# Performance work log

Measured on AMD Instinct MI355X. Metric: run time of the kernel, lower is better.

The kernel has to match this reference:

```python
import jax, jax.numpy as jnp
import numpy as np

B, N, D = 512, 256, 16   # batch, tokens (num_patches+1), embed_dim (= n_qubits)
STAGES = 4               # log2(D) butterfly stages


def _safe_acos(u):
    # matches torch acos + nan_to_num: out-of-range -> 0, with clean gradients
    ok = jnp.abs(u) <= 1.0
    return jnp.where(ok, jnp.arccos(jnp.clip(u, -1.0, 1.0)), 0.0)


def get_rbs_parameters(x):
    # x: [B, N, D] -> RBS angles [B, N, D-1]; recursive spherical-coordinate decomposition
    a0 = _safe_acos(x[..., 0])
    def step(carry, xi):
        t, a_prev = carry
        inv = jnp.nan_to_num(1.0 / jnp.sin(a_prev))
        t = t * inv
        a = _safe_acos(xi * t)
        return (t, a), a
    xs = jnp.moveaxis(x[..., 1:D - 1], -1, 0)  # [D-2, B, N]
    _, rest = jax.lax.scan(step, (jnp.ones_like(a0), a0), xs)
    alphas = jnp.concatenate([a0[None], rest], axis=0)  # [D-1, B, N]
    return jnp.moveaxis(alphas, 0, -1)


def amplitudes(alphas):
    # unary-state amplitudes prepared by the diagonal vector loader
    # a_i = cos(alpha_i) * prod_{k<i} sin(alpha_k);  a_{D-1} = prod_k sin(alpha_k)
    sins = jnp.sin(alphas)
    prefix = jnp.concatenate([jnp.ones_like(sins[..., :1]), jnp.cumprod(sins, axis=-1)], axis=-1)  # [B,N,D]
    return jnp.concatenate([prefix[..., :D - 1] * jnp.cos(alphas), prefix[..., D - 1:]], axis=-1)


def butterfly_matrix(angles):
    # orthogonal DxD matrix implemented by the Butterfly RBS circuit in the unary subspace
    d = 2 * angles.shape[1]
    M = jnp.eye(d, dtype=angles.dtype)
    for s in range(angles.shape[0]):
        step = 1 << s
        idx_i = np.array([i for i in range(d) if (i // step) % 2 == 0])
        idx_j = idx_i + step
        c = jnp.cos(angles[s])[:, None]
        sn = jnp.sin(angles[s])[:, None]
        Mi, Mj = M[idx_i], M[idx_j]
        M = M.at[idx_i].set(c * Mi + sn * Mj)
        M = M.at[idx_j].set(-sn * Mi + c * Mj)
    return M


def layer_norm(x, g, b, eps=1e-5):
    mu = jnp.mean(x, -1, keepdims=True)
    var = jnp.var(x, -1, keepdims=True)
    return (x - mu) / jnp.sqrt(var + eps) * g + b


def setup_inputs() -> dict:
    key = jax.random.key(0)
    ks = jax.random.split(key, 4)
    return {
        "x": jax.random.normal(ks[0], (B, N, D), jnp.float32),
        "ln1_g": jnp.ones((D,), jnp.float32),
        "ln1_b": jnp.zeros((D,), jnp.float32),
        "angles": jax.random.normal(ks[1], (STAGES, D // 2), jnp.float32),
        "ln2_g": jnp.ones((D,), jnp.float32),
        "ln2_b": jnp.zeros((D,), jnp.float32),
        "w1": jax.random.normal(ks[2], (D, 4 * D), jnp.float32) / np.sqrt(D).astype(np.float32),
        "b1": jnp.zeros((4 * D,), jnp.float32),
        "w2": jax.random.normal(ks[3], (4 * D, D), jnp.float32) / np.sqrt(4 * D).astype(np.float32),
        "b2": jnp.zeros((D,), jnp.float32),
    }


def reference(x, ln1_g, ln1_b, angles, ln2_g, ln2_b, w1, b1, w2, b2):
    inp = layer_norm(x, ln1_g, ln1_b) / 2.0
    alphas = jnp.nan_to_num(get_rbs_parameters(inp))
    a = amplitudes(alphas)                 # [B,N,D] loaded unary amplitudes
    W = butterfly_matrix(angles)           # [D,D] orthogonal butterfly
    Wa = jnp.einsum('de,bne->bnd', W, a)   # [B,N,D]
    vxT = jnp.abs(Wa)
    # xwx[b,i,j] = sqrt(P(qubit0=1)) = |<a_j| W |a_i>| for the xWx circuit
    xwx = jnp.abs(jnp.einsum('bid,bjd->bij', Wa, a))
    attn = jax.nn.softmax(xwx, axis=-1)
    x = x + jnp.einsum('bij,bjd->bid', attn, vxT)
    h = layer_norm(x, ln2_g, ln2_b)
    h = jax.nn.gelu(h @ w1 + b1, approximate=False) @ w2 + b2
    return x + h
```

## Files before the change

### kernel.cpp

```cpp
#include <hip/hip_runtime.h>
#include <math.h>

#define NTOK 256
#define DD 16
#define BDIM 512

typedef short short8 __attribute__((ext_vector_type(8)));
typedef float f32x16 __attribute__((ext_vector_type(16)));
typedef unsigned int u32;
typedef unsigned long long u64;

__device__ __forceinline__ u32 f2bf(float f) {
    u32 u = __float_as_uint(f);
    u += 0x7FFFu + ((u >> 16) & 1u);
    return u >> 16;
}
struct U128 { u64 a, b; };
__device__ __forceinline__ short8 ld8(const unsigned short* p) {
    U128 t;
    t.a = *(const u64*)(p);
    t.b = *(const u64*)(p + 4);
    return __builtin_bit_cast(short8, t);
}
__device__ __forceinline__ void pack_swap16(f32x16 p, short8& f0, short8& f1) {
    u32 W00, W01, W10, W11, W20, W21, W30, W31;
    asm("v_cvt_pk_bf16_f32 %0, %1, %2" : "=v"(W00) : "v"(p[0]),  "v"(p[1]));
    asm("v_cvt_pk_bf16_f32 %0, %1, %2" : "=v"(W01) : "v"(p[2]),  "v"(p[3]));
    asm("v_cvt_pk_bf16_f32 %0, %1, %2" : "=v"(W10) : "v"(p[4]),  "v"(p[5]));
    asm("v_cvt_pk_bf16_f32 %0, %1, %2" : "=v"(W11) : "v"(p[6]),  "v"(p[7]));
    asm("v_cvt_pk_bf16_f32 %0, %1, %2" : "=v"(W20) : "v"(p[8]),  "v"(p[9]));
    asm("v_cvt_pk_bf16_f32 %0, %1, %2" : "=v"(W21) : "v"(p[10]), "v"(p[11]));
    asm("v_cvt_pk_bf16_f32 %0, %1, %2" : "=v"(W30) : "v"(p[12]), "v"(p[13]));
    asm("v_cvt_pk_bf16_f32 %0, %1, %2" : "=v"(W31) : "v"(p[14]), "v"(p[15]));
    asm("v_permlane32_swap_b32 %0, %1" : "+v"(W00), "+v"(W10));
    asm("v_permlane32_swap_b32 %0, %1" : "+v"(W01), "+v"(W11));
    asm("v_permlane32_swap_b32 %0, %1" : "+v"(W20), "+v"(W30));
    asm("v_permlane32_swap_b32 %0, %1" : "+v"(W21), "+v"(W31));
    struct { u32 x, y, z, w; } i0{W00, W01, W10, W11}, i1{W20, W21, W30, W31};
    f0 = __builtin_bit_cast(short8, i0);
    f1 = __builtin_bit_cast(short8, i1);
}
__device__ __forceinline__ float gelu_erf(float v) {
    float xx = v * 0.70710678118654752f;
    float ax = fabsf(xx);
    float t = __builtin_amdgcn_rcpf(__builtin_fmaf(0.3275911f, ax, 1.0f));
    float poly = t * (0.254829592f + t * (-0.284496736f + t * (1.421413741f
               + t * (-1.453152027f + t * 1.061405429f))));
    float r = 1.0f - poly * __expf(-ax * ax);
    float e = copysignf(r, xx);
    return 0.5f * v * (1.0f + e);
}

__global__ __launch_bounds__(BDIM, 4) void qab_kernel(
    const float* __restrict__ x,
    const float* __restrict__ ln1_g, const float* __restrict__ ln1_b,
    const float* __restrict__ angles,
    const float* __restrict__ ln2_g, const float* __restrict__ ln2_b,
    const float* __restrict__ w1, const float* __restrict__ b1,
    const float* __restrict__ w2, const float* __restrict__ b2,
    float* __restrict__ out)
{
    __shared__ alignas(16) unsigned short a_bf[NTOK][20];
    __shared__ alignas(16) unsigned short wa_bf[NTOK][20];
    __shared__ alignas(16) unsigned short vxT[17][268];
    __shared__ alignas(16) unsigned short w1tb[64][20];
    __shared__ alignas(16) unsigned short w2tb[16][68];
    __shared__ alignas(16) float b1_lds[64];
    __shared__ alignas(16) float ln2g_lds[DD];
    __shared__ alignas(16) float ln2b_lds[DD];
    __shared__ alignas(16) float b2_lds[DD];

    const int b    = blockIdx.x;
    const int tid  = threadIdx.x;
    const int r    = tid & (NTOK - 1);
    const int q    = tid >> 8;
    const int w    = tid >> 6;
    const int l31  = tid & 31;
    const int hi   = (tid >> 5) & 1;
    const int lane = tid & 63;

    const float* xres = x + ((size_t)b * NTOK + 32 * w + l31) * DD;
    const float4 xra = *(const float4*)(xres + 4 * hi);
    const float4 xrb = *(const float4*)(xres + 8 + 4 * hi);

    f32x16 zc;
    #pragma unroll
    for (int t = 0; t < 16; ++t) zc[t] = 0.0f;

    float amp[DD];
    {
        const float* xrow = x + ((size_t)b * NTOK + r) * DD;
        float xr[DD];
        #pragma unroll
        for (int qq = 0; qq < 4; ++qq) {
            float4 v = ((const float4*)xrow)[qq];
            xr[4*qq+0] = v.x; xr[4*qq+1] = v.y; xr[4*qq+2] = v.z; xr[4*qq+3] = v.w;
        }
        float mu = 0.0f;
        #pragma unroll
        for (int d = 0; d < DD; ++d) mu += xr[d];
        mu *= (1.0f / DD);
        float var = 0.0f;
        #pragma unroll
        for (int d = 0; d < DD; ++d) { float dv = xr[d] - mu; var += dv * dv; }
        var *= (1.0f / DD);
        float rs = 1.0f / sqrtf(var + 1e-5f);
        float inp[DD];
        #pragma unroll
        for (int d = 0; d < DD; ++d)
            inp[d] = ((xr[d] - mu) * rs * ln1_g[d] + ln1_b[d]) * 0.5f;

        float P = 1.0f;
        #pragma unroll
        for (int i = 0; i < DD - 1; ++i) {
            float v = inp[i];
            float v2 = v * v;
            bool ok = v2 <= P;
            amp[i] = ok ? v : __builtin_amdgcn_sqrtf(P);
            P = ok ? __builtin_fmaf(-v, v, P) : 0.0f;
        }
        amp[DD - 1] = __builtin_amdgcn_sqrtf(P);
    }

    if (q == 0) {
        u32 aw[8];
        #pragma unroll
        for (int k = 0; k < 8; ++k)
            asm("v_cvt_pk_bf16_f32 %0, %1, %2" : "=v"(aw[k]) : "v"(amp[2*k]), "v"(amp[2*k+1]));
        *(u64*)&a_bf[r][0]  = (u64)aw[0] | ((u64)aw[1] << 32);
        *(u64*)&a_bf[r][4]  = (u64)aw[2] | ((u64)aw[3] << 32);
        *(u64*)&a_bf[r][8]  = (u64)aw[4] | ((u64)aw[5] << 32);
        *(u64*)&a_bf[r][12] = (u64)aw[6] | ((u64)aw[7] << 32);
        for (int i = r; i < 64 * DD; i += NTOK) {
            w1tb[i & 63][i >> 6] = (unsigned short)f2bf(w1[i]);
            w2tb[i & 15][i >> 4] = (unsigned short)f2bf(w2[i]);
        }
        if (r >= 128 && r < 192) b1_lds[r - 128] = b1[r - 128];
        if (r >= 192 && r < 208) ln2g_lds[r - 192] = ln2_g[r - 192];
        if (r >= 208 && r < 224) ln2b_lds[r - 208] = ln2_b[r - 208];
        if (r >= 224 && r < 240) b2_lds[r - 224] = b2[r - 224];
        vxT[16][r] = 0x3F80;
    } else {
        float sn_l = 0.0f, cs_l = 0.0f;
        if (lane < 32) __sincosf(angles[lane], &sn_l, &cs_l);
        #pragma unroll
        for (int s = 0; s < 4; ++s) {
            const int step = 1 << s;
            #pragma unroll
            for (int p = 0; p < 8; ++p) {
                const int i = ((p >> s) << (s + 1)) | (p & (step - 1));
                const int j = i + step;
                float sn = __shfl(sn_l, s * 8 + p, 64);
                float cs = __shfl(cs_l, s * 8 + p, 64);
                float vi = amp[i], vj = amp[j];
                amp[i] =  cs * vi + sn * vj;
                amp[j] = -sn * vi + cs * vj;
            }
        }
        u32 ww[8];
        #pragma unroll
        for (int k = 0; k < 8; ++k)
            asm("v_cvt_pk_bf16_f32 %0, %1, %2" : "=v"(ww[k]) : "v"(amp[2*k]), "v"(amp[2*k+1]));
        *(u64*)&wa_bf[r][0]  = (u64)ww[0] | ((u64)ww[1] << 32);
        *(u64*)&wa_bf[r][4]  = (u64)ww[2] | ((u64)ww[3] << 32);
        *(u64*)&wa_bf[r][8]  = (u64)ww[4] | ((u64)ww[5] << 32);
        *(u64*)&wa_bf[r][12] = (u64)ww[6] | ((u64)ww[7] << 32);
        #pragma unroll
        for (int d = 0; d < DD; ++d)
            vxT[d][r] = (unsigned short)f2bf(fabsf(amp[d]));
    }
    __syncthreads();

    const int ncl = (l31 < 16) ? l31 : 16;
    f32x16 Oacc = zc;
    {
        short8 waf = ld8(&wa_bf[w * 32 + l31][8 * hi]);
        short8 af[8];
        #pragma unroll
        for (int jt = 0; jt < 8; ++jt)
            af[jt] = ld8(&a_bf[jt * 32 + l31][8 * hi]);
        short8 va0 = ld8(&vxT[ncl][8 * hi]);
        short8 va1 = ld8(&vxT[ncl][16 + 8 * hi]);
        f32x16 S0 = __builtin_amdgcn_mfma_f32_32x32x16_bf16(af[0], waf, zc, 0, 0, 0);
        #pragma unroll
        for (int jt = 0; jt < 8; ++jt) {
            f32x16 Sn;
            if (jt < 7)
                Sn = __builtin_amdgcn_mfma_f32_32x32x16_bf16(af[jt + 1], waf, zc, 0, 0, 0);
            short8 nva0, nva1;
            if (jt < 7) {
                nva0 = ld8(&vxT[ncl][(jt + 1) * 32 + 8 * hi]);
                nva1 = ld8(&vxT[ncl][(jt + 1) * 32 + 16 + 8 * hi]);
            }
            f32x16 pv;
            #pragma unroll
            for (int t = 0; t < 16; ++t) pv[t] = __expf(fabsf(S0[t]));
            short8 pb0, pb1;
            pack_swap16(pv, pb0, pb1);
            Oacc = __builtin_amdgcn_mfma_f32_32x32x16_bf16(va0, pb0, Oacc, 0, 0, 0);
            Oacc = __builtin_amdgcn_mfma_f32_32x32x16_bf16(va1, pb1, Oacc, 0, 0, 0);
            S0 = Sn; va0 = nva0; va1 = nva1;
        }
    }

    const float rl = 1.0f / Oacc[8];
    float o1[8];
    o1[0] = xra.x + Oacc[0] * rl;  o1[1] = xra.y + Oacc[1] * rl;
    o1[2] = xra.z + Oacc[2] * rl;  o1[3] = xra.w + Oacc[3] * rl;
    o1[4] = xrb.x + Oacc[4] * rl;  o1[5] = xrb.y + Oacc[5] * rl;
    o1[6] = xrb.z + Oacc[6] * rl;  o1[7] = xrb.w + Oacc[7] * rl;

    float s8 = 0.0f;
    #pragma unroll
    for (int t = 0; t < 8; ++t) s8 += o1[t];
    float mu2 = (s8 + __shfl_xor(s8, 32, 64)) * (1.0f / DD);
    float v8 = 0.0f;
    #pragma unroll
    for (int t = 0; t < 8; ++t) { float dv = o1[t] - mu2; v8 += dv * dv; }
    float var2 = (v8 + __shfl_xor(v8, 32, 64)) * (1.0f / DD);
    float rs2 = 1.0f / sqrtf(var2 + 1e-5f);

    const float4 g0v = *(const float4*)&ln2g_lds[4 * hi];
    const float4 g1v = *(const float4*)&ln2g_lds[8 + 4 * hi];
    const float4 bb0 = *(const float4*)&ln2b_lds[4 * hi];
    const float4 bb1 = *(const float4*)&ln2b_lds[8 + 4 * hi];
    float h[8];
    h[0] = (o1[0]-mu2)*rs2*g0v.x + bb0.x;  h[1] = (o1[1]-mu2)*rs2*g0v.y + bb0.y;
    h[2] = (o1[2]-mu2)*rs2*g0v.z + bb0.z;  h[3] = (o1[3]-mu2)*rs2*g0v.w + bb0.w;
    h[4] = (o1[4]-mu2)*rs2*g1v.x + bb1.x;  h[5] = (o1[5]-mu2)*rs2*g1v.y + bb1.y;
    h[6] = (o1[6]-mu2)*rs2*g1v.z + bb1.z;  h[7] = (o1[7]-mu2)*rs2*g1v.w + bb1.w;

    short8 hB;
    {
        u32 w0, w1u, w2u, w3;
        asm("v_cvt_pk_bf16_f32 %0, %1, %2" : "=v"(w0)  : "v"(h[0]), "v"(h[1]));
        asm("v_cvt_pk_bf16_f32 %0, %1, %2" : "=v"(w1u) : "v"(h[2]), "v"(h[3]));
        asm("v_cvt_pk_bf16_f32 %0, %1, %2" : "=v"(w2u) : "v"(h[4]), "v"(h[5]));
        asm("v_cvt_pk_bf16_f32 %0, %1, %2" : "=v"(w3)  : "v"(h[6]), "v"(h[7]));
        asm("s_nop 1\n\tv_permlane32_swap_b32 %0, %1" : "+v"(w0),  "+v"(w2u));
        asm("s_nop 1\n\tv_permlane32_swap_b32 %0, %1" : "+v"(w1u), "+v"(w3));
        struct { u32 x, y, z, w; } hw{w0, w1u, w2u, w3};
        hB = __builtin_bit_cast(short8, hw);
    }

    const int dcl = (l31 < 15) ? l31 : 15;
    f32x16 O2 = zc;
    {
        const float4 c0 = *(const float4*)&b2_lds[4 * hi];
        const float4 c1 = *(const float4*)&b2_lds[8 + 4 * hi];
        O2[0] = c0.x; O2[1] = c0.y; O2[2] = c0.z; O2[3] = c0.w;
        O2[4] = c1.x; O2[5] = c1.y; O2[6] = c1.z; O2[7] = c1.w;
    }
    {
        f32x16 Hc0, Hc1;
        #pragma unroll
        for (int kblk = 0; kblk < 2; ++kblk) {
            const float* bp = &b1_lds[32 * kblk];
            const float4 c0 = *(const float4*)(bp + 4 * hi);
            const float4 c1 = *(const float4*)(bp + 8 + 4 * hi);
            const float4 c2 = *(const float4*)(bp + 16 + 4 * hi);
            const float4 c3 = *(const float4*)(bp + 24 + 4 * hi);
            f32x16& Hc = kblk ? Hc1 : Hc0;
            Hc[0]=c0.x; Hc[1]=c0.y; Hc[2]=c0.z; Hc[3]=c0.w;
            Hc[4]=c1.x; Hc[5]=c1.y; Hc[6]=c1.z; Hc[7]=c1.w;
            Hc[8]=c2.x; Hc[9]=c2.y; Hc[10]=c2.z; Hc[11]=c2.w;
            Hc[12]=c3.x; Hc[13]=c3.y; Hc[14]=c3.z; Hc[15]=c3.w;
        }
        short8 w1f0 = ld8(&w1tb[l31][8 * hi]);
        short8 w1f1 = ld8(&w1tb[32 + l31][8 * hi]);
        short8 w2a0 = ld8(&w2tb[dcl][8 * hi]);
        short8 w2a1 = ld8(&w2tb[dcl][16 + 8 * hi]);
        short8 w2b0 = ld8(&w2tb[dcl][32 + 8 * hi]);
        short8 w2b1 = ld8(&w2tb[dcl][48 + 8 * hi]);
        f32x16 H0 = __builtin_amdgcn_mfma_f32_32x32x16_bf16(w1f0, hB, Hc0, 0, 0, 0);
        f32x16 H1 = __builtin_amdgcn_mfma_f32_32x32x16_bf16(w1f1, hB, Hc1, 0, 0, 0);
        f32x16 gv0, gv1;
        #pragma unroll
        for (int t = 0; t < 16; ++t) gv0[t] = gelu_erf(H0[t]);
        short8 ga0, ga1;
        pack_swap16(gv0, ga0, ga1);
        #pragma unroll
        for (int t = 0; t < 16; ++t) gv1[t] = gelu_erf(H1[t]);
        short8 gb0, gb1;
        pack_swap16(gv1, gb0, gb1);
        O2 = __builtin_amdgcn_mfma_f32_32x32x16_bf16(w2a0, ga0, O2, 0, 0, 0);
        O2 = __builtin_amdgcn_mfma_f32_32x32x16_bf16(w2a1, ga1, O2, 0, 0, 0);
        O2 = __builtin_amdgcn_mfma_f32_32x32x16_bf16(w2b0, gb0, O2, 0, 0, 0);
        O2 = __builtin_amdgcn_mfma_f32_32x32x16_bf16(w2b1, gb1, O2, 0, 0, 0);
    }

    {
        float* orow = out + ((size_t)b * NTOK + 32 * w + l31) * DD;
        float4 oa, ob;
        oa.x = o1[0] + O2[0]; oa.y = o1[1] + O2[1];
        oa.z = o1[2] + O2[2]; oa.w = o1[3] + O2[3];
        ob.x = o1[4] + O2[4]; ob.y = o1[5] + O2[5];
        ob.z = o1[6] + O2[6]; ob.w = o1[7] + O2[7];
        *(float4*)(orow + 4 * hi) = oa;
        *(float4*)(orow + 8 + 4 * hi) = ob;
    }
}

extern "C" void kernel_launch(void* const* d_in, const int* in_sizes, int n_in,
                              void* d_out, int out_size, void* d_ws, size_t ws_size,
                              hipStream_t stream) {
    const float* x     = (const float*)d_in[0];
    const float* ln1_g = (const float*)d_in[1];
    const float* ln1_b = (const float*)d_in[2];
    const float* ang   = (const float*)d_in[3];
    const float* ln2_g = (const float*)d_in[4];
    const float* ln2_b = (const float*)d_in[5];
    const float* w1    = (const float*)d_in[6];
    const float* b1    = (const float*)d_in[7];
    const float* w2    = (const float*)d_in[8];
    const float* b2    = (const float*)d_in[9];
    float* out = (float*)d_out;

    const int B = in_sizes[0] / (NTOK * DD);
    hipLaunchKernelGGL(qab_kernel, dim3(B), dim3(BDIM), 0, stream,
                       x, ln1_g, ln1_b, ang, ln2_g, ln2_b, w1, b1, w2, b2, out);
}
```

Measured before the change: 19.95 us.

## Split LayerNorm and amplitude prep into a separate kernel via workspace

Moves the per-token LayerNorm and amplitude-loading computation into its own kernel, which writes bf16 amplitudes to a global workspace. The main kernel then loads them instead of recomputing them in both halves of the block, so the duplicated prep work goes away. The butterfly half now applies its rotations to bf16-rounded amplitudes rather than fp32, which changes precision. The cost is a second launch plus a global write and read round trip of the amplitudes.

```diff
diff --git a/kernel.cpp b/kernel.cpp
--- a/kernel.cpp
+++ b/kernel.cpp
@@ -14,6 +14,9 @@
     u32 u = __float_as_uint(f);
     u += 0x7FFFu + ((u >> 16) & 1u);
     return u >> 16;
+}
+__device__ __forceinline__ float bf2f(unsigned short h) {
+    return __uint_as_float(((u32)h) << 16);
 }
 struct U128 { u64 a, b; };
 __device__ __forceinline__ short8 ld8(const unsigned short* p) {
@@ -51,13 +54,66 @@
     return 0.5f * v * (1.0f + e);
 }
 
-__global__ __launch_bounds__(BDIM, 4) void qab_kernel(
+__global__ __launch_bounds__(256, 8) void qab_prep(
     const float* __restrict__ x,
     const float* __restrict__ ln1_g, const float* __restrict__ ln1_b,
+    u64* __restrict__ a_g)
+{
+    const size_t row = (size_t)blockIdx.x * 256 + threadIdx.x;
+    const float* xrow = x + row * DD;
+    float xr[DD];
+    #pragma unroll
+    for (int qq = 0; qq < 4; ++qq) {
+        float4 v = ((const float4*)xrow)[qq];
+        xr[4*qq+0] = v.x; xr[4*qq+1] = v.y; xr[4*qq+2] = v.z; xr[4*qq+3] = v.w;
+    }
+    float mu = 0.0f;
+    #pragma unroll
+    for (int d = 0; d < DD; ++d) mu += xr[d];
+    mu *= (1.0f / DD);
+    float var = 0.0f;
+    #pragma unroll
+    for (int d = 0; d < DD; ++d) { float dv = xr[d] - mu; var += dv * dv; }
+    var *= (1.0f / DD);
+    float rs = 1.0f / sqrtf(var + 1e-5f);
+    float inp[DD];
+    #pragma unroll
+    for (int d = 0; d < DD; ++d)
+        inp[d] = ((xr[d] - mu) * rs * ln1_g[d] + ln1_b[d]) * 0.5f;
+
+    float amp[DD];
+    float P = 1.0f;
+    #pragma unroll
+    for (int i = 0; i < DD - 1; ++i) {
+        float v = inp[i];
+        float v2 = v * v;
+        bool ok = v2 <= P;
+        amp[i] = ok ? v : __builtin_amdgcn_sqrtf(P);
+        P = ok ? __builtin_fmaf(-v, v, P) : 0.0f;
+    }
+    amp[DD - 1] = __builtin_amdgcn_sqrtf(P);
+
+    u32 aw[8];
+    #pragma unroll
+    for (int k = 0; k < 8; ++k)
+        asm("v_cvt_pk_bf16_f32 %0, %1, %2" : "=v"(aw[k]) : "v"(amp[2*k]), "v"(amp[2*k+1]));
+    ulonglong2 v0, v1;
+    v0.x = (u64)aw[0] | ((u64)aw[1] << 32);
+    v0.y = (u64)aw[2] | ((u64)aw[3] << 32);
+    v1.x = (u64)aw[4] | ((u64)aw[5] << 32);
+    v1.y = (u64)aw[6] | ((u64)aw[7] << 32);
+    u64* dst = a_g + row * 4;
+    *(ulonglong2*)(dst)     = v0;
+    *(ulonglong2*)(dst + 2) = v1;
+}
+
+__global__ __launch_bounds__(BDIM, 4) void qab_main(
+    const float* __restrict__ x,
     const float* __restrict__ angles,
     const float* __restrict__ ln2_g, const float* __restrict__ ln2_b,
     const float* __restrict__ w1, const float* __restrict__ b1,
     const float* __restrict__ w2, const float* __restrict__ b2,
+    const u64* __restrict__ a_g,
     float* __restrict__ out)
 {
     __shared__ alignas(16) unsigned short a_bf[NTOK][20];
@@ -87,50 +143,15 @@
     #pragma unroll
     for (int t = 0; t < 16; ++t) zc[t] = 0.0f;
 
-    float amp[DD];
-    {
-        const float* xrow = x + ((size_t)b * NTOK + r) * DD;
-        float xr[DD];
-        #pragma unroll
-        for (int qq = 0; qq < 4; ++qq) {
-            float4 v = ((const float4*)xrow)[qq];
-            xr[4*qq+0] = v.x; xr[4*qq+1] = v.y; xr[4*qq+2] = v.z; xr[4*qq+3] = v.w;
-        }
-        float mu = 0.0f;
-        #pragma unroll
-        for (int d = 0; d < DD; ++d) mu += xr[d];
-        mu *= (1.0f / DD);
-        float var = 0.0f;
-        #pragma unroll
-        for (int d = 0; d < DD; ++d) { float dv = xr[d] - mu; var += dv * dv; }
-        var *= (1.0f / DD);
-        float rs = 1.0f / sqrtf(var + 1e-5f);
-        float inp[DD];
-        #pragma unroll
-        for (int d = 0; d < DD; ++d)
-            inp[d] = ((xr[d] - mu) * rs * ln1_g[d] + ln1_b[d]) * 0.5f;
-
-        float P = 1.0f;
-        #pragma unroll
-        for (int i = 0; i < DD - 1; ++i) {
-            float v = inp[i];
-            float v2 = v * v;
-            bool ok = v2 <= P;
-            amp[i] = ok ? v : __builtin_amdgcn_sqrtf(P);
-            P = ok ? __builtin_fmaf(-v, v, P) : 0.0f;
-        }
-        amp[DD - 1] = __builtin_amdgcn_sqrtf(P);
-    }
+    const u64* src = a_g + ((size_t)b * NTOK + r) * 4;
+    const ulonglong2 t0 = *(const ulonglong2*)(src);
+    const ulonglong2 t1 = *(const ulonglong2*)(src + 2);
 
     if (q == 0) {
-        u32 aw[8];
-        #pragma unroll
-        for (int k = 0; k < 8; ++k)
-            asm("v_cvt_pk_bf16_f32 %0, %1, %2" : "=v"(aw[k]) : "v"(amp[2*k]), "v"(amp[2*k+1]));
-        *(u64*)&a_bf[r][0]  = (u64)aw[0] | ((u64)aw[1] << 32);
-        *(u64*)&a_bf[r][4]  = (u64)aw[2] | ((u64)aw[3] << 32);
-        *(u64*)&a_bf[r][8]  = (u64)aw[4] | ((u64)aw[5] << 32);
-        *(u64*)&a_bf[r][12] = (u64)aw[6] | ((u64)aw[7] << 32);
+        *(u64*)&a_bf[r][0]  = t0.x;
+        *(u64*)&a_bf[r][4]  = t0.y;
+        *(u64*)&a_bf[r][8]  = t1.x;
+        *(u64*)&a_bf[r][12] = t1.y;
         for (int i = r; i < 64 * DD; i += NTOK) {
             w1tb[i & 63][i >> 6] = (unsigned short)f2bf(w1[i]);
             w2tb[i & 15][i >> 4] = (unsigned short)f2bf(w2[i]);
@@ -141,6 +162,15 @@
         if (r >= 224 && r < 240) b2_lds[r - 224] = b2[r - 224];
         vxT[16][r] = 0x3F80;
     } else {
+        float amp[DD];
+        {
+            u64 words[4] = { t0.x, t0.y, t1.x, t1.y };
+            #pragma unroll
+            for (int j = 0; j < 4; ++j)
+                #pragma unroll
+                for (int e = 0; e < 4; ++e)
+                    amp[4*j + e] = bf2f((unsigned short)(words[j] >> (16 * e)));
+        }
         float sn_l = 0.0f, cs_l = 0.0f;
         if (lane < 32) __sincosf(angles[lane], &sn_l, &cs_l);
         #pragma unroll
@@ -317,6 +347,10 @@
     float* out = (float*)d_out;
 
     const int B = in_sizes[0] / (NTOK * DD);
-    hipLaunchKernelGGL(qab_kernel, dim3(B), dim3(BDIM), 0, stream,
-                       x, ln1_g, ln1_b, ang, ln2_g, ln2_b, w1, b1, w2, b2, out);
-}
+    u64* a_g = (u64*)d_ws;
+
+    hipLaunchKernelGGL(qab_prep, dim3(B), dim3(256), 0, stream,
+                       x, ln1_g, ln1_b, a_g);
+    hipLaunchKernelGGL(qab_main, dim3(B), dim3(BDIM), 0, stream,
+                       x, ang, ln2_g, ln2_b, w1, b1, w2, b2, a_g, out);
+}
```

After: 24.23 us. 21.4% more time.
